# Kernel tuning notes

Hardware: AMD Instinct MI355X
Metric: run time of the kernel (lower is better)

Reference implementation:

```python
import jax, jax.numpy as jnp
import numpy as np
import math

N, D, E, M, MODS = 16384, 1024, 5, 64, 5
K = 1  # top-k for sparse router


def setup_inputs() -> dict:
    key = jax.random.key(0)
    ks = jax.random.split(key, 24)
    rn = lambda k, shape, s=1.0: jax.random.normal(k, shape, dtype=jnp.float32) * s
    inp = {
        'x': rn(ks[0], (N, D)),
        'spectrogram': rn(ks[1], (N, D)),
        'waveform': rn(ks[2], (N, D)),
        'pitch': rn(ks[3], (N, D)),
        'envelope': rn(ks[4], (N, D)),
        'phase': rn(ks[5], (N, D)),
        # routers (torch Linear: y = x @ W.T + b, W is [out,in]); init std=0.01
        'Wsoft': rn(ks[6], (E, D), 0.01), 'bsoft': jnp.zeros((E,), jnp.float32),
        'Wsparse': rn(ks[7], (E, D), 0.01), 'bsparse': jnp.zeros((E,), jnp.float32),
        # memory (plain randn, not re-initialized)
        'm_key': rn(ks[8], (M, D)), 'm_val': rn(ks[9], (M, E)),
        # experts: Linear(D,D) -> SiLU -> Linear(D,D), stacked over E
        'W1': rn(ks[10], (E, D, D), 0.01), 'b1': jnp.zeros((E, D), jnp.float32),
        'W2': rn(ks[11], (E, D, D), 0.01), 'b2': jnp.zeros((E, D), jnp.float32),
        # fusion gates: Linear(D,1) + sigmoid, one per modality
        'Wg': rn(ks[12], (MODS, D), 0.01), 'bg': jnp.zeros((MODS,), jnp.float32),
        # fusion projection: Linear(D*MODS, D)
        'Wf': rn(ks[13], (D, D * MODS), 0.01), 'bf': jnp.zeros((D,), jnp.float32),
    }
    return inp


def reference(x, spectrogram, waveform, pitch, envelope, phase,
              Wsoft, bsoft, Wsparse, bsparse, m_key, m_val,
              W1, b1, W2, b2, Wg, bg, Wf, bf):
    alpha_moe = jnp.float32(0.5)
    alpha_fusion = jnp.float32(0.5)

    # soft router: softmax(Linear)
    soft_w = jax.nn.softmax(x @ Wsoft.T + bsoft, axis=-1)          # [N,E]

    # sparse router: top-k + softmax, scattered back to [N,E]
    logits = x @ Wsparse.T + bsparse                               # [N,E]
    top_vals, top_idx = jax.lax.top_k(logits, K)                   # [N,K]
    sparse_gates = jax.nn.softmax(top_vals, axis=-1)               # [N,K]
    one_hot = jax.nn.one_hot(top_idx, E, dtype=logits.dtype)       # [N,K,E]
    sparse_w = jnp.sum(one_hot * sparse_gates[..., None], axis=1)  # [N,E]

    # memory-augmented gating
    attn = jax.nn.softmax((x @ m_key.T) / math.sqrt(D), axis=-1)   # [N,M]
    memory_w = jax.nn.softmax(attn @ m_val, axis=-1)               # [N,E]

    mixed_w = alpha_moe * sparse_w + (1 - alpha_moe) * soft_w
    final_w = (mixed_w + memory_w) / 2                             # [N,E]

    # dense all-expert MLP: [N,E,D]
    h = jax.nn.silu(jnp.einsum('nd,eod->neo', x, W1) + b1)
    expert_out = jnp.einsum('ned,eod->neo', h, W2) + b2
    moe_output = jnp.einsum('neo,ne->no', expert_out, final_w)     # [N,D]

    # gated multimodal fusion
    features = [spectrogram, waveform, pitch, envelope, phase]
    gates = jax.nn.sigmoid(x @ Wg.T + bg)                          # [N,MODS]
    scaled = [gates[:, q:q + 1] * features[q] for q in range(MODS)]
    fused = jnp.concatenate(scaled, axis=-1) @ Wf.T + bf           # [N,D]

    return alpha_fusion * fused + (1 - alpha_fusion) * moe_output
```

## Files before the change

kernel.cpp:

```cpp
#include <hip/hip_runtime.h>
#include <stdint.h>

typedef __bf16 bf16x8 __attribute__((ext_vector_type(8)));
typedef float f32x4 __attribute__((ext_vector_type(4)));
typedef unsigned short u16;
typedef u16 ushort8 __attribute__((ext_vector_type(8)));
typedef u16 ushort4v __attribute__((ext_vector_type(4)));

__device__ __forceinline__ u16 f2bf(float f) {
    uint32_t u = __builtin_bit_cast(uint32_t, f);
    u += 0x7FFFu + ((u >> 16) & 1u);
    return (u16)(u >> 16);
}

__device__ __forceinline__ void gload16(const void* g, void* l) {
    __builtin_amdgcn_global_load_lds(
        reinterpret_cast<const __attribute__((address_space(1))) void*>(reinterpret_cast<uintptr_t>(g)),
        reinterpret_cast<__attribute__((address_space(3))) void*>(reinterpret_cast<uintptr_t>(l)),
        16, 0, 0);
}

#define BAR() asm volatile("s_barrier" ::: "memory")
#define SGBi(m, n) __builtin_amdgcn_sched_group_barrier((m), (n), 0)

template <int V>
__device__ __forceinline__ void sgb_q() {
    SGBi(0x70, V);
    SGBi(0x8, 2); SGBi(0x100, 1);
    SGBi(0x8, 2); SGBi(0x100, 1);
    SGBi(0x8, 2); SGBi(0x100, 1);
    SGBi(0x8, 2); SGBi(0x100, 1);
    SGBi(0x8, 8);
}
__device__ __forceinline__ void sgb_q3() {
    SGBi(0x70, 2);
    SGBi(0x8, 1); SGBi(0x100, 1);
    SGBi(0x8, 1); SGBi(0x100, 1);
    SGBi(0x8, 1); SGBi(0x100, 1);
    SGBi(0x8, 1); SGBi(0x100, 1);
    SGBi(0x8, 12);
    SGBi(0x100, 8);
}

template <int MODE>
__global__ __launch_bounds__(512, 2)
void gemm256(const u16* __restrict__ A, int lda,
             const u16* __restrict__ B, int ldb, int K,
             void* __restrict__ Cout, int ldc,
             const float* __restrict__ bias, const float* __restrict__ fw05,
             const float* __restrict__ g05,
             const float* __restrict__ f0, const float* __restrict__ f1,
             const float* __restrict__ f2, const float* __restrict__ f3,
             const float* __restrict__ f4)
{
    __shared__ __align__(16) u16 As[2 * 256 * 64];
    __shared__ __align__(16) u16 Bs[2 * 256 * 64];

    const int t    = threadIdx.x;
    const int lane = t & 63;
    const int wave = t >> 6;
    const int l16  = lane & 15;
    const int lhi  = lane >> 4;
    const int wm   = wave >> 2;
    const int wn   = wave & 3;

    const int gx  = gridDim.x;
    const int nwg = gx * gridDim.y;
    int id  = blockIdx.y * gx + blockIdx.x;
    int swz = (nwg & 7) ? id : ((id & 7) * (nwg >> 3) + (id >> 3));
    const int bx = swz % gx;
    const int by = swz / gx;

    const size_t rowBase = (size_t)by * 256;
    const int    colBase = bx * 256;
    const int    NT      = K >> 6;

    const int rl0 = t >> 3;
    const int ko0 = (t & 7) * 8;
    const int kos = ((t & 7) ^ (rl0 & 7)) * 8;

    const u16* aRow = A + (rowBase + rl0) * (size_t)lda + kos;
    const u16* bRow = B + (size_t)(colBase + rl0) * ldb + kos;
    u16* asW = As + rl0 * 64 + ko0;
    u16* bsW = Bs + rl0 * 64 + ko0;

#define STA(bufo, e, r0, r1)                                                     \
    do {                                                                         \
        gload16(aRow + (size_t)(r0) * lda + (e), asW + (bufo) + (r0) * 64);      \
        gload16(aRow + (size_t)(r1) * lda + (e), asW + (bufo) + (r1) * 64);      \
    } while (0)
#define STB(bufo, e, b0)                                                         \
    do {                                                                         \
        gload16(bRow + (size_t)(b0) * ldb + (e), bsW + (bufo) + (b0) * 64);      \
        gload16(bRow + (size_t)((b0) + 64) * ldb + (e),                          \
                bsW + (bufo) + ((b0) + 64) * 64);                                \
    } while (0)

    const int sw = l16 & 7;
    const u16* aRd0 = As + (wm * 128 + l16) * 64 + ((lhi ^ sw) * 8);
    const u16* aRd1 = As + (wm * 128 + l16) * 64 + (((lhi + 4) ^ sw) * 8);
    const u16* bRd0 = Bs + (wn * 64 + l16) * 64 + ((lhi ^ sw) * 8);
    const u16* bRd1 = Bs + (wn * 64 + l16) * 64 + (((lhi + 4) ^ sw) * 8);

#define RDAF(dst, cc, qq)                                                        \
    do {                                                                         \
        dst[0][0] = *(const bf16x8*)(aRd0 + (cc) + (2 * (qq) + 0) * 1024);       \
        dst[0][1] = *(const bf16x8*)(aRd1 + (cc) + (2 * (qq) + 0) * 1024);       \
        dst[1][0] = *(const bf16x8*)(aRd0 + (cc) + (2 * (qq) + 1) * 1024);       \
        dst[1][1] = *(const bf16x8*)(aRd1 + (cc) + (2 * (qq) + 1) * 1024);       \
    } while (0)
#define RDB(cc)                                                                  \
    do {                                                                         \
        _Pragma("unroll")                                                        \
        for (int ni = 0; ni < 4; ++ni) {                                         \
            bfr[ni][0] = *(const bf16x8*)(bRd0 + (cc) + ni * 1024);              \
            bfr[ni][1] = *(const bf16x8*)(bRd1 + (cc) + ni * 1024);              \
        }                                                                        \
    } while (0)
#define MMX(af, r0)                                                              \
    do {                                                                         \
        __builtin_amdgcn_s_setprio(1);                                           \
        _Pragma("unroll")                                                        \
        for (int s = 0; s < 2; ++s)                                              \
            _Pragma("unroll")                                                    \
            for (int ni = 0; ni < 4; ++ni)                                       \
                _Pragma("unroll")                                                \
                for (int kk = 0; kk < 2; ++kk)                                   \
                    acc[(r0) + s][ni] = __builtin_amdgcn_mfma_f32_16x16x32_bf16( \
                        af[s][kk], bfr[ni][kk], acc[(r0) + s][ni], 0, 0, 0);     \
        __builtin_amdgcn_s_setprio(0);                                           \
    } while (0)

    f32x4 acc[8][4];
#pragma unroll
    for (int i = 0; i < 8; i++)
#pragma unroll
        for (int j = 0; j < 4; j++)
            acc[i][j] = (f32x4){0.f, 0.f, 0.f, 0.f};

    const float* fsrc = nullptr;
    int   dbase = 0;
    f32x4 bl0 = {0.f, 0.f, 0.f, 0.f}, bl1 = {0.f, 0.f, 0.f, 0.f};
    float bgd = 0.f;
    if constexpr (MODE == 0) {
        const int qm = bx >> 2;
        fsrc  = (qm == 0) ? f0 : (qm == 1) ? f1 : (qm == 2) ? f2 : (qm == 3) ? f3 : f4;
        dbase = (bx & 3) * 256;
        const int br = t >> 5, bc = (t & 31) * 8;
        bl0 = *(const f32x4*)(fsrc + (rowBase + br) * 1024 + dbase + bc);
        bl1 = *(const f32x4*)(fsrc + (rowBase + br) * 1024 + dbase + bc + 4);
        bgd = g05[(rowBase + br) * 5 + (bx >> 2)];
    }

    STA(0, 0, 0, 128);
    STA(0, 0, 64, 192);
    STB(0, 0, 0);
    STB(0, 0, 128);
    STB(16384, 64, 0);
    STB(16384, 64, 128);
    STA(16384, 64, 0, 128);
    asm volatile("s_waitcnt vmcnt(6)" ::: "memory");
    BAR();

    bf16x8 afA[2][2], afB[2][2], bfr[4][2];
    RDAF(afA, 0, 0);
    RDB(0);

    for (int tt = 0; tt < NT; ++tt) {
        const int c  = (tt & 1) << 14;
        const int cn = c ^ 16384;
        const int e1 = ((tt + 1 < NT) ? tt + 1 : NT - 1) << 6;
        const int e2 = ((tt + 2 < NT) ? tt + 2 : NT - 1) << 6;

        if constexpr (MODE == 0) {
            const int idx = tt * 512 + t;
            const int br  = idx >> 5;
            const int bc  = (idx & 31) * 8;
            ushort8 bv;
            bv[0] = f2bf(bgd * bl0[0]); bv[1] = f2bf(bgd * bl0[1]);
            bv[2] = f2bf(bgd * bl0[2]); bv[3] = f2bf(bgd * bl0[3]);
            bv[4] = f2bf(bgd * bl1[0]); bv[5] = f2bf(bgd * bl1[1]);
            bv[6] = f2bf(bgd * bl1[2]); bv[7] = f2bf(bgd * bl1[3]);
            *(ushort8*)((u16*)Cout + (rowBase + br) * (size_t)ldc
                        + 5184 + colBase + bc) = bv;
            const int t2   = (tt + 1 < 16) ? tt + 1 : 15;
            const int idx2 = t2 * 512 + t;
            const int br2  = idx2 >> 5;
            const int bc2  = (idx2 & 31) * 8;
            bl0 = *(const f32x4*)(fsrc + (rowBase + br2) * 1024 + dbase + bc2);
            bl1 = *(const f32x4*)(fsrc + (rowBase + br2) * 1024 + dbase + bc2 + 4);
            bgd = g05[(rowBase + br2) * 5 + (bx >> 2)];
        }
        STA(cn, e1, 64, 192);
        RDAF(afB, c, 1);
        MMX(afA, 0);
        sgb_q<(MODE == 0) ? 6 : 2>();
        BAR();

        STB(c, e2, 0);
        RDAF(afA, c, 2);
        MMX(afB, 2);
        sgb_q<2>();
        BAR();

        STB(c, e2, 128);
        RDAF(afB, c, 3);
        MMX(afA, 4);
        sgb_q<2>();
        asm volatile("s_waitcnt vmcnt(4)" ::: "memory");
        BAR();

        STA(c, e2, 0, 128);
        RDAF(afA, cn, 0);
        MMX(afB, 6);
        RDB(cn);
        sgb_q3();
        BAR();
    }

    const int orow = wm * 128 + lhi * 4;
    const int ocol = colBase + wn * 64 + l16;

    if constexpr (MODE == 0) {
        u16* C = (u16*)Cout;
        const int eidx = colBase >> 10;
#pragma unroll
        for (int mi = 0; mi < 8; mi++) {
#pragma unroll
            for (int j = 0; j < 4; j++) {
                size_t r = rowBase + orow + mi * 16 + j;
                float w = fw05[r * 5 + eidx];
#pragma unroll
                for (int ni = 0; ni < 4; ni++) {
                    int cc = ocol + ni * 16;
                    float v = acc[mi][ni][j] + bias[cc];
                    float s = v / (1.f + __expf(-v));
                    C[r * (size_t)ldc + cc] = f2bf(w * s);
                }
            }
        }
    } else {
        float* C = (float*)Cout;
#pragma unroll
        for (int mi = 0; mi < 8; mi++) {
#pragma unroll
            for (int j = 0; j < 4; j++) {
                size_t r = rowBase + orow + mi * 16 + j;
#pragma unroll
                for (int ni = 0; ni < 4; ni++) {
                    size_t idx = r * (size_t)ldc + (ocol + ni * 16);
                    C[idx] = acc[mi][ni][j];
                }
            }
        }
    }
#undef STA
#undef STB
#undef RDAF
#undef RDB
#undef MMX
}

__global__ __launch_bounds__(256)
void router_kernel(const float* __restrict__ x,
                   const float* __restrict__ Wsoft, const float* __restrict__ Wsparse,
                   const float* __restrict__ m_key, const float* __restrict__ Wg,
                   float* __restrict__ logits, u16* __restrict__ Xbf)
{
    __shared__ float Xs[128][66];
    __shared__ float Ws[80][132];

    const int t    = threadIdx.x;
    const int lane = t & 63;
    const int wave = t >> 6;
    const int row0 = blockIdx.x * 64;

    float acc[20];
#pragma unroll
    for (int c = 0; c < 20; c++) acc[c] = 0.f;

    for (int k0 = 0; k0 < 1024; k0 += 128) {
#pragma unroll
        for (int i = 0; i < 8; i++) {
            int f4 = i * 256 + t;
            int r  = f4 >> 5;
            int kk = (f4 & 31) * 4;
            f32x4 v = *(const f32x4*)(x + (size_t)(row0 + r) * 1024 + k0 + kk);
            Xs[kk + 0][r] = v[0]; Xs[kk + 1][r] = v[1];
            Xs[kk + 2][r] = v[2]; Xs[kk + 3][r] = v[3];
            ushort4v o4;
            o4[0] = f2bf(v[0]); o4[1] = f2bf(v[1]);
            o4[2] = f2bf(v[2]); o4[3] = f2bf(v[3]);
            *(ushort4v*)(Xbf + (size_t)(row0 + r) * 1024 + k0 + kk) = o4;
        }
#pragma unroll
        for (int i = 0; i < 10; i++) {
            int f4 = i * 256 + t;
            int j  = f4 >> 5;
            int kk = (f4 & 31) * 4;
            const float* src;
            if      (j < 5)  src = Wsoft   + (size_t)j * 1024;
            else if (j < 10) src = Wsparse + (size_t)(j - 5) * 1024;
            else if (j < 74) src = m_key   + (size_t)(j - 10) * 1024;
            else             src = Wg      + (size_t)(j - 74) * 1024;
            *(f32x4*)&Ws[j][kk] = *(const f32x4*)(src + k0 + kk);
        }
        __syncthreads();

        for (int k4 = 0; k4 < 32; k4++) {
            float x0 = Xs[k4 * 4 + 0][lane];
            float x1 = Xs[k4 * 4 + 1][lane];
            float x2 = Xs[k4 * 4 + 2][lane];
            float x3 = Xs[k4 * 4 + 3][lane];
#pragma unroll
            for (int c = 0; c < 20; c++) {
                f32x4 w = *(const f32x4*)&Ws[wave * 20 + c][k4 * 4];
                acc[c] += x0 * w[0] + x1 * w[1] + x2 * w[2] + x3 * w[3];
            }
        }
        __syncthreads();
    }

    float* dst = logits + (size_t)(row0 + lane) * 80 + wave * 20;
#pragma unroll
    for (int c = 0; c < 20; c++) dst[c] = acc[c];
}

__global__ __launch_bounds__(256)
void finalize_kernel(const float* __restrict__ logits, const float* __restrict__ m_val,
                     const float* __restrict__ bsoft, const float* __restrict__ bsparse,
                     const float* __restrict__ bg,
                     float* __restrict__ fw05, float* __restrict__ g05,
                     u16* __restrict__ Abuf, int NC)
{
    __shared__ float mv[320];
    for (int i = threadIdx.x; i < 320; i += 256) mv[i] = m_val[i];
    __syncthreads();

    int idx = blockIdx.x * 256 + threadIdx.x;
    if (idx >= NC) return;
    const float* L = logits + (size_t)idx * 80;

    float sl[5];
#pragma unroll
    for (int e = 0; e < 5; e++) sl[e] = L[e] + bsoft[e];
    float sm = sl[0];
#pragma unroll
    for (int e = 1; e < 5; e++) sm = fmaxf(sm, sl[e]);
    float ssum = 0.f, sw[5];
#pragma unroll
    for (int e = 0; e < 5; e++) { sw[e] = __expf(sl[e] - sm); ssum += sw[e]; }
    float sinv = 1.f / ssum;

    int am = 0; float bv = L[5] + bsparse[0];
#pragma unroll
    for (int e = 1; e < 5; e++) {
        float v = L[5 + e] + bsparse[e];
        if (v > bv) { bv = v; am = e; }
    }

    float amax = -1e30f;
    for (int m = 0; m < 64; m++) amax = fmaxf(amax, L[10 + m] * 0.03125f);
    float asum = 0.f, mw[5] = {0.f, 0.f, 0.f, 0.f, 0.f};
    for (int m = 0; m < 64; m++) {
        float a = __expf(L[10 + m] * 0.03125f - amax);
        asum += a;
#pragma unroll
        for (int e = 0; e < 5; e++) mw[e] += a * mv[m * 5 + e];
    }
    float ainv = 1.f / asum;
#pragma unroll
    for (int e = 0; e < 5; e++) mw[e] *= ainv;
    float mm = mw[0];
#pragma unroll
    for (int e = 1; e < 5; e++) mm = fmaxf(mm, mw[e]);
    float msum = 0.f, me[5];
#pragma unroll
    for (int e = 0; e < 5; e++) { me[e] = __expf(mw[e] - mm); msum += me[e]; }
    float minv = 1.f / msum;

    u16* ta = Abuf + (size_t)idx * 10368;
#pragma unroll
    for (int e = 0; e < 5; e++) {
        float fv = 0.125f * ((e == am) ? 1.f : 0.f) + 0.125f * sw[e] * sinv
                 + 0.25f * me[e] * minv;
        fw05[(size_t)idx * 5 + e] = fv;
        ta[5120 + e] = f2bf(fv);
    }
#pragma unroll
    for (int q = 0; q < 5; q++)
        g05[(size_t)idx * 5 + q] = 0.5f / (1.f + __expf(-(L[74 + q] + bg[q])));

    for (int j = 5125; j < 5184; j++) ta[j] = 0;
    ta[10304] = f2bf(0.5f);
    for (int j = 10305; j < 10368; j++) ta[j] = 0;
}

__global__ __launch_bounds__(256)
void cast_bf16_kernel(const float* __restrict__ src, u16* __restrict__ dst, size_t n)
{
    size_t i = ((size_t)blockIdx.x * 256 + threadIdx.x) * 8;
    if (i >= n) return;
    f32x4 a = *(const f32x4*)(src + i);
    f32x4 b = *(const f32x4*)(src + i + 4);
    ushort8 o;
    o[0] = f2bf(a[0]); o[1] = f2bf(a[1]); o[2] = f2bf(a[2]); o[3] = f2bf(a[3]);
    o[4] = f2bf(b[0]); o[5] = f2bf(b[1]); o[6] = f2bf(b[2]); o[7] = f2bf(b[3]);
    *(ushort8*)(dst + i) = o;
}

__global__ __launch_bounds__(256)
void prep_wcat(const float* __restrict__ W2, const float* __restrict__ b2,
               const float* __restrict__ Wf, const float* __restrict__ bfias,
               u16* __restrict__ out)
{
    size_t tid = (size_t)blockIdx.x * 256 + threadIdx.x;
    int o  = (int)(tid / 1296);
    int c0 = (int)(tid % 1296) * 8;
    ushort8 v;
    if (c0 + 8 <= 5120) {
        int e = c0 >> 10, d = c0 & 1023;
        const float* s = W2 + ((size_t)e * 1024 + o) * 1024 + d;
        f32x4 a = *(const f32x4*)s;
        f32x4 b = *(const f32x4*)(s + 4);
        v[0] = f2bf(a[0]); v[1] = f2bf(a[1]); v[2] = f2bf(a[2]); v[3] = f2bf(a[3]);
        v[4] = f2bf(b[0]); v[5] = f2bf(b[1]); v[6] = f2bf(b[2]); v[7] = f2bf(b[3]);
    } else if (c0 < 5184) {
#pragma unroll
        for (int jj = 0; jj < 8; jj++) {
            int c = c0 + jj;
            float f = (c >= 5120 && c < 5125) ? b2[(size_t)(c - 5120) * 1024 + o] : 0.f;
            v[jj] = f2bf(f);
        }
    } else {
        int c2 = c0 - 5184;
        if (c2 + 8 <= 5120) {
            const float* s = Wf + (size_t)o * 5120 + c2;
            f32x4 a = *(const f32x4*)s;
            f32x4 b = *(const f32x4*)(s + 4);
            v[0] = f2bf(a[0]); v[1] = f2bf(a[1]); v[2] = f2bf(a[2]); v[3] = f2bf(a[3]);
            v[4] = f2bf(b[0]); v[5] = f2bf(b[1]); v[6] = f2bf(b[2]); v[7] = f2bf(b[3]);
        } else {
#pragma unroll
            for (int jj = 0; jj < 8; jj++) {
                int cj = c2 + jj;
                v[jj] = f2bf((cj == 5120) ? bfias[o] : 0.f);
            }
        }
    }
    *(ushort8*)(out + (size_t)o * 10368 + c0) = v;
}

extern "C" void kernel_launch(void* const* d_in, const int* in_sizes, int n_in,
                              void* d_out, int out_size, void* d_ws, size_t ws_size,
                              hipStream_t stream)
{
    (void)in_sizes; (void)n_in; (void)out_size;

    const float* x      = (const float*)d_in[0];
    const float* spect  = (const float*)d_in[1];
    const float* wavef  = (const float*)d_in[2];
    const float* pitch  = (const float*)d_in[3];
    const float* envel  = (const float*)d_in[4];
    const float* phase  = (const float*)d_in[5];
    const float* Wsoft  = (const float*)d_in[6];
    const float* bsoft  = (const float*)d_in[7];
    const float* Wsparse= (const float*)d_in[8];
    const float* bsparse= (const float*)d_in[9];
    const float* m_key  = (const float*)d_in[10];
    const float* m_val  = (const float*)d_in[11];
    const float* W1     = (const float*)d_in[12];
    const float* b1     = (const float*)d_in[13];
    const float* W2     = (const float*)d_in[14];
    const float* b2     = (const float*)d_in[15];
    const float* Wg     = (const float*)d_in[16];
    const float* bg     = (const float*)d_in[17];
    const float* Wf     = (const float*)d_in[18];
    const float* bfias  = (const float*)d_in[19];
    float* out = (float*)d_out;

    const int N = 16384;

    size_t fixed = (size_t)5 * 1024 * 1024 * 2 + (size_t)1024 * 10368 * 2;
    int NC = 16384;
    while (NC > 256 && fixed + (size_t)NC * 23144 > ws_size) NC >>= 1;

    char* p = (char*)d_ws;
    u16* W1bf = (u16*)p; p += (size_t)5 * 1024 * 1024 * 2;
    u16* Wcat = (u16*)p; p += (size_t)1024 * 10368 * 2;
    u16* Xbf  = (u16*)p; p += (size_t)NC * 1024 * 2;
    u16* Abuf = (u16*)p; p += (size_t)NC * 10368 * 2;
    float* logits = (float*)p; p += (size_t)NC * 80 * 4;
    float* fw05   = (float*)p; p += (size_t)NC * 5 * 4;
    float* g05    = (float*)p; p += (size_t)NC * 5 * 4;

    cast_bf16_kernel<<<2560, 256, 0, stream>>>(W1, W1bf, (size_t)5 * 1024 * 1024);
    prep_wcat<<<5184, 256, 0, stream>>>(W2, b2, Wf, bfias, Wcat);

    for (int n0 = 0; n0 < N; n0 += NC) {
        const size_t off = (size_t)n0 * 1024;

        router_kernel<<<NC / 64, 256, 0, stream>>>(x + off, Wsoft, Wsparse, m_key, Wg,
                                                   logits, Xbf);
        finalize_kernel<<<(NC + 255) / 256, 256, 0, stream>>>(
            logits, m_val, bsoft, bsparse, bg, fw05, g05, Abuf, NC);

        gemm256<0><<<dim3(20, NC / 256), 512, 0, stream>>>(
            Xbf, 1024, W1bf, 1024, 1024, Abuf, 10368, b1, fw05, g05,
            spect + off, wavef + off, pitch + off, envel + off, phase + off);

        gemm256<1><<<dim3(4, NC / 256), 512, 0, stream>>>(
            Abuf, 10368, Wcat, 10368, 10368, out + off, 1024,
            nullptr, nullptr, nullptr, nullptr, nullptr, nullptr, nullptr, nullptr);
    }
}
```

Baseline: 665.7 us.

## Offload modality gate-scale copy to dedicated producer waves in first GEMM

Splits the templated GEMM into two kernels. In the first, two extra waves (640 threads per block) convert the gated modality features to bf16 and write them into the concatenated activation buffer, work that the MFMA waves previously interleaved into their main loop. The extra waves join every block barrier so they stay in step with the GEMM waves. This takes global loads and stores off the MFMA waves' critical path, but launch bounds fall from two blocks per CU to one, which cuts occupancy and may raise register pressure.

After: 1.307 ms. 1.96x slower.

```diff
diff --git a/kernel.cpp b/kernel.cpp
--- a/kernel.cpp
+++ b/kernel.cpp
@@ -42,27 +42,19 @@
     SGBi(0x100, 8);
 }
 
-template <int MODE>
-__global__ __launch_bounds__(512, 2)
-void gemm256(const u16* __restrict__ A, int lda,
-             const u16* __restrict__ B, int ldb, int K,
-             void* __restrict__ Cout, int ldc,
-             const float* __restrict__ bias, const float* __restrict__ fw05,
-             const float* __restrict__ g05,
-             const float* __restrict__ f0, const float* __restrict__ f1,
-             const float* __restrict__ f2, const float* __restrict__ f3,
-             const float* __restrict__ f4)
+__global__ __launch_bounds__(640, 1)
+void gemm_moe(const u16* __restrict__ A, const u16* __restrict__ B,
+              u16* __restrict__ C, const float* __restrict__ bias,
+              const float* __restrict__ fw05, const float* __restrict__ g05,
+              const float* __restrict__ f0, const float* __restrict__ f1,
+              const float* __restrict__ f2, const float* __restrict__ f3,
+              const float* __restrict__ f4)
 {
     __shared__ __align__(16) u16 As[2 * 256 * 64];
     __shared__ __align__(16) u16 Bs[2 * 256 * 64];
 
     const int t    = threadIdx.x;
-    const int lane = t & 63;
     const int wave = t >> 6;
-    const int l16  = lane & 15;
-    const int lhi  = lane >> 4;
-    const int wm   = wave >> 2;
-    const int wn   = wave & 3;
 
     const int gx  = gridDim.x;
     const int nwg = gx * gridDim.y;
@@ -73,34 +65,44 @@
 
     const size_t rowBase = (size_t)by * 256;
     const int    colBase = bx * 256;
-    const int    NT      = K >> 6;
-
-    const int rl0 = t >> 3;
-    const int ko0 = (t & 7) * 8;
-    const int kos = ((t & 7) ^ (rl0 & 7)) * 8;
-
-    const u16* aRow = A + (rowBase + rl0) * (size_t)lda + kos;
-    const u16* bRow = B + (size_t)(colBase + rl0) * ldb + kos;
-    u16* asW = As + rl0 * 64 + ko0;
-    u16* bsW = Bs + rl0 * 64 + ko0;
+    const int    qm      = bx >> 2;
+    const float* fq = (qm == 0) ? f0 : (qm == 1) ? f1 : (qm == 2) ? f2
+                      : (qm == 3) ? f3 : f4;
+    const int dbase = (bx & 3) * 256;
+
+    if (wave < 8) {
+        const int lane = t & 63;
+        const int l16  = lane & 15;
+        const int lhi  = lane >> 4;
+        const int wm   = wave >> 2;
+        const int wn   = wave & 3;
+
+        const int rl0 = t >> 3;
+        const int ko0 = (t & 7) * 8;
+        const int kos = ((t & 7) ^ (rl0 & 7)) * 8;
+
+        const u16* aRow = A + (rowBase + rl0) * (size_t)1024 + kos;
+        const u16* bRow = B + (size_t)(colBase + rl0) * 1024 + kos;
+        u16* asW = As + rl0 * 64 + ko0;
+        u16* bsW = Bs + rl0 * 64 + ko0;
 
 #define STA(bufo, e, r0, r1)                                                     \
     do {                                                                         \
-        gload16(aRow + (size_t)(r0) * lda + (e), asW + (bufo) + (r0) * 64);      \
-        gload16(aRow + (size_t)(r1) * lda + (e), asW + (bufo) + (r1) * 64);      \
+        gload16(aRow + (size_t)(r0) * 1024 + (e), asW + (bufo) + (r0) * 64);     \
+        gload16(aRow + (size_t)(r1) * 1024 + (e), asW + (bufo) + (r1) * 64);     \
     } while (0)
 #define STB(bufo, e, b0)                                                         \
     do {                                                                         \
-        gload16(bRow + (size_t)(b0) * ldb + (e), bsW + (bufo) + (b0) * 64);      \
-        gload16(bRow + (size_t)((b0) + 64) * ldb + (e),                          \
+        gload16(bRow + (size_t)(b0) * 1024 + (e), bsW + (bufo) + (b0) * 64);     \
+        gload16(bRow + (size_t)((b0) + 64) * 1024 + (e),                         \
                 bsW + (bufo) + ((b0) + 64) * 64);                                \
     } while (0)
 
-    const int sw = l16 & 7;
-    const u16* aRd0 = As + (wm * 128 + l16) * 64 + ((lhi ^ sw) * 8);
-    const u16* aRd1 = As + (wm * 128 + l16) * 64 + (((lhi + 4) ^ sw) * 8);
-    const u16* bRd0 = Bs + (wn * 64 + l16) * 64 + ((lhi ^ sw) * 8);
-    const u16* bRd1 = Bs + (wn * 64 + l16) * 64 + (((lhi + 4) ^ sw) * 8);
+        const int sw = l16 & 7;
+        const u16* aRd0 = As + (wm * 128 + l16) * 64 + ((lhi ^ sw) * 8);
+        const u16* aRd1 = As + (wm * 128 + l16) * 64 + (((lhi + 4) ^ sw) * 8);
+        const u16* bRd0 = Bs + (wn * 64 + l16) * 64 + ((lhi ^ sw) * 8);
+        const u16* bRd1 = Bs + (wn * 64 + l16) * 64 + (((lhi + 4) ^ sw) * 8);
 
 #define RDAF(dst, cc, qq)                                                        \
     do {                                                                         \
@@ -131,26 +133,200 @@
         __builtin_amdgcn_s_setprio(0);                                           \
     } while (0)
 
+        f32x4 acc[8][4];
+#pragma unroll
+        for (int i = 0; i < 8; i++)
+#pragma unroll
+            for (int j = 0; j < 4; j++)
+                acc[i][j] = (f32x4){0.f, 0.f, 0.f, 0.f};
+
+        STA(0, 0, 0, 128);
+        STA(0, 0, 64, 192);
+        STB(0, 0, 0);
+        STB(0, 0, 128);
+        STB(16384, 64, 0);
+        STB(16384, 64, 128);
+        STA(16384, 64, 0, 128);
+        asm volatile("s_waitcnt vmcnt(6)" ::: "memory");
+        BAR();
+
+        bf16x8 afA[2][2], afB[2][2], bfr[4][2];
+        RDAF(afA, 0, 0);
+        RDB(0);
+
+        for (int tt = 0; tt < 16; ++tt) {
+            const int c  = (tt & 1) << 14;
+            const int cn = c ^ 16384;
+            const int e1 = ((tt + 1 < 16) ? tt + 1 : 15) << 6;
+            const int e2 = ((tt + 2 < 16) ? tt + 2 : 15) << 6;
+
+            STA(cn, e1, 64, 192);
+            RDAF(afB, c, 1);
+            MMX(afA, 0);
+            sgb_q<2>();
+            BAR();
+            STB(c, e2, 0);
+            RDAF(afA, c, 2);
+            MMX(afB, 2);
+            sgb_q<2>();
+            BAR();
+            STB(c, e2, 128);
+            RDAF(afB, c, 3);
+            MMX(afA, 4);
+            sgb_q<2>();
+            asm volatile("s_waitcnt vmcnt(4)" ::: "memory");
+            BAR();
+            STA(c, e2, 0, 128);
+            RDAF(afA, cn, 0);
+            MMX(afB, 6);
+            RDB(cn);
+            sgb_q3();
+            BAR();
+        }
+
+        const int orow = wm * 128 + lhi * 4;
+        const int ocol = colBase + wn * 64 + l16;
+#pragma unroll
+        for (int mi = 0; mi < 8; mi++) {
+#pragma unroll
+            for (int j = 0; j < 4; j++) {
+                size_t r = rowBase + orow + mi * 16 + j;
+                float w = fw05[r * 5 + qm];
+#pragma unroll
+                for (int ni = 0; ni < 4; ni++) {
+                    int cc = ocol + ni * 16;
+                    float v = acc[mi][ni][j] + bias[cc];
+                    float s = v / (1.f + __expf(-v));
+                    C[r * (size_t)10368 + cc] = f2bf(w * s);
+                }
+            }
+        }
+#undef STA
+#undef STB
+#undef RDAF
+#undef RDB
+#undef MMX
+    } else {
+        const int bt   = t - 512;
+        const int rof  = bt >> 5;
+        const int bcol = (bt & 31) * 8;
+
+        size_t r0 = rowBase + rof;
+        f32x4 la  = *(const f32x4*)(fq + r0 * 1024 + dbase + bcol);
+        f32x4 lb  = *(const f32x4*)(fq + r0 * 1024 + dbase + bcol + 4);
+        float lg  = g05[r0 * 5 + qm];
+        size_t rcur = r0;
+
+        BAR();
+
+        for (int s = 0; s < 64; ++s) {
+            ushort8 v;
+            v[0] = f2bf(lg * la[0]); v[1] = f2bf(lg * la[1]);
+            v[2] = f2bf(lg * la[2]); v[3] = f2bf(lg * la[3]);
+            v[4] = f2bf(lg * lb[0]); v[5] = f2bf(lg * lb[1]);
+            v[6] = f2bf(lg * lb[2]); v[7] = f2bf(lg * lb[3]);
+            *(ushort8*)(C + rcur * 10368 + 5184 + colBase + bcol) = v;
+
+            const int s2 = (s + 1 < 64) ? s + 1 : 63;
+            size_t rn = rowBase + s2 * 4 + rof;
+            la = *(const f32x4*)(fq + rn * 1024 + dbase + bcol);
+            lb = *(const f32x4*)(fq + rn * 1024 + dbase + bcol + 4);
+            lg = g05[rn * 5 + qm];
+            rcur = rn;
+            BAR();
+        }
+    }
+}
+
+__global__ __launch_bounds__(512, 2)
+void gemm_out(const u16* __restrict__ A, int lda,
+              const u16* __restrict__ B, int ldb, int K,
+              float* __restrict__ C, int ldc)
+{
+    __shared__ __align__(16) u16 As[2 * 256 * 64];
+    __shared__ __align__(16) u16 Bs[2 * 256 * 64];
+
+    const int t    = threadIdx.x;
+    const int lane = t & 63;
+    const int wave = t >> 6;
+    const int l16  = lane & 15;
+    const int lhi  = lane >> 4;
+    const int wm   = wave >> 2;
+    const int wn   = wave & 3;
+
+    const int gx  = gridDim.x;
+    const int nwg = gx * gridDim.y;
+    int id  = blockIdx.y * gx + blockIdx.x;
+    int swz = (nwg & 7) ? id : ((id & 7) * (nwg >> 3) + (id >> 3));
+    const int bx = swz % gx;
+    const int by = swz / gx;
+
+    const size_t rowBase = (size_t)by * 256;
+    const int    colBase = bx * 256;
+    const int    NT      = K >> 6;
+
+    const int rl0 = t >> 3;
+    const int ko0 = (t & 7) * 8;
+    const int kos = ((t & 7) ^ (rl0 & 7)) * 8;
+
+    const u16* aRow = A + (rowBase + rl0) * (size_t)lda + kos;
+    const u16* bRow = B + (size_t)(colBase + rl0) * ldb + kos;
+    u16* asW = As + rl0 * 64 + ko0;
+    u16* bsW = Bs + rl0 * 64 + ko0;
+
+#define STA(bufo, e, r0, r1)                                                     \
+    do {                                                                         \
+        gload16(aRow + (size_t)(r0) * lda + (e), asW + (bufo) + (r0) * 64);      \
+        gload16(aRow + (size_t)(r1) * lda + (e), asW + (bufo) + (r1) * 64);      \
+    } while (0)
+#define STB(bufo, e, b0)                                                         \
+    do {                                                                         \
+        gload16(bRow + (size_t)(b0) * ldb + (e), bsW + (bufo) + (b0) * 64);      \
+        gload16(bRow + (size_t)((b0) + 64) * ldb + (e),                          \
+                bsW + (bufo) + ((b0) + 64) * 64);                                \
+    } while (0)
+
+    const int sw = l16 & 7;
+    const u16* aRd0 = As + (wm * 128 + l16) * 64 + ((lhi ^ sw) * 8);
+    const u16* aRd1 = As + (wm * 128 + l16) * 64 + (((lhi + 4) ^ sw) * 8);
+    const u16* bRd0 = Bs + (wn * 64 + l16) * 64 + ((lhi ^ sw) * 8);
+    const u16* bRd1 = Bs + (wn * 64 + l16) * 64 + (((lhi + 4) ^ sw) * 8);
+
+#define RDAF(dst, cc, qq)                                                        \
+    do {                                                                         \
+        dst[0][0] = *(const bf16x8*)(aRd0 + (cc) + (2 * (qq) + 0) * 1024);       \
+        dst[0][1] = *(const bf16x8*)(aRd1 + (cc) + (2 * (qq) + 0) * 1024);       \
+        dst[1][0] = *(const bf16x8*)(aRd0 + (cc) + (2 * (qq) + 1) * 1024);       \
+        dst[1][1] = *(const bf16x8*)(aRd1 + (cc) + (2 * (qq) + 1) * 1024);       \
+    } while (0)
+#define RDB(cc)                                                                  \
+    do {                                                                         \
+        _Pragma("unroll")                                                        \
+        for (int ni = 0; ni < 4; ++ni) {                                         \
+            bfr[ni][0] = *(const bf16x8*)(bRd0 + (cc) + ni * 1024);              \
+            bfr[ni][1] = *(const bf16x8*)(bRd1 + (cc) + ni * 1024);              \
+        }                                                                        \
+    } while (0)
+#define MMX(af, r0)                                                              \
+    do {                                                                         \
+        __builtin_amdgcn_s_setprio(1);                                           \
+        _Pragma("unroll")                                                        \
+        for (int s = 0; s < 2; ++s)                                              \
+            _Pragma("unroll")                                                    \
+            for (int ni = 0; ni < 4; ++ni)                                       \
+                _Pragma("unroll")                                                \
+                for (int kk = 0; kk < 2; ++kk)                                   \
+                    acc[(r0) + s][ni] = __builtin_amdgcn_mfma_f32_16x16x32_bf16( \
+                        af[s][kk], bfr[ni][kk], acc[(r0) + s][ni], 0, 0, 0);     \
+        __builtin_amdgcn_s_setprio(0);                                           \
+    } while (0)
+
     f32x4 acc[8][4];
 #pragma unroll
     for (int i = 0; i < 8; i++)
 #pragma unroll
         for (int j = 0; j < 4; j++)
             acc[i][j] = (f32x4){0.f, 0.f, 0.f, 0.f};
-
-    const float* fsrc = nullptr;
-    int   dbase = 0;
-    f32x4 bl0 = {0.f, 0.f, 0.f, 0.f}, bl1 = {0.f, 0.f, 0.f, 0.f};
-    float bgd = 0.f;
-    if constexpr (MODE == 0) {
-        const int qm = bx >> 2;
-        fsrc  = (qm == 0) ? f0 : (qm == 1) ? f1 : (qm == 2) ? f2 : (qm == 3) ? f3 : f4;
-        dbase = (bx & 3) * 256;
-        const int br = t >> 5, bc = (t & 31) * 8;
-        bl0 = *(const f32x4*)(fsrc + (rowBase + br) * 1024 + dbase + bc);
-        bl1 = *(const f32x4*)(fsrc + (rowBase + br) * 1024 + dbase + bc + 4);
-        bgd = g05[(rowBase + br) * 5 + (bx >> 2)];
-    }
 
     STA(0, 0, 0, 128);
     STA(0, 0, 64, 192);
@@ -172,29 +348,10 @@
         const int e1 = ((tt + 1 < NT) ? tt + 1 : NT - 1) << 6;
         const int e2 = ((tt + 2 < NT) ? tt + 2 : NT - 1) << 6;
 
-        if constexpr (MODE == 0) {
-            const int idx = tt * 512 + t;
-            const int br  = idx >> 5;
-            const int bc  = (idx & 31) * 8;
-            ushort8 bv;
-            bv[0] = f2bf(bgd * bl0[0]); bv[1] = f2bf(bgd * bl0[1]);
-            bv[2] = f2bf(bgd * bl0[2]); bv[3] = f2bf(bgd * bl0[3]);
-            bv[4] = f2bf(bgd * bl1[0]); bv[5] = f2bf(bgd * bl1[1]);
-            bv[6] = f2bf(bgd * bl1[2]); bv[7] = f2bf(bgd * bl1[3]);
-            *(ushort8*)((u16*)Cout + (rowBase + br) * (size_t)ldc
-                        + 5184 + colBase + bc) = bv;
-            const int t2   = (tt + 1 < 16) ? tt + 1 : 15;
-            const int idx2 = t2 * 512 + t;
-            const int br2  = idx2 >> 5;
-            const int bc2  = (idx2 & 31) * 8;
-            bl0 = *(const f32x4*)(fsrc + (rowBase + br2) * 1024 + dbase + bc2);
-            bl1 = *(const f32x4*)(fsrc + (rowBase + br2) * 1024 + dbase + bc2 + 4);
-            bgd = g05[(rowBase + br2) * 5 + (bx >> 2)];
-        }
         STA(cn, e1, 64, 192);
         RDAF(afB, c, 1);
         MMX(afA, 0);
-        sgb_q<(MODE == 0) ? 6 : 2>();
+        sgb_q<2>();
         BAR();
 
         STB(c, e2, 0);
@@ -220,37 +377,15 @@
 
     const int orow = wm * 128 + lhi * 4;
     const int ocol = colBase + wn * 64 + l16;
-
-    if constexpr (MODE == 0) {
-        u16* C = (u16*)Cout;
-        const int eidx = colBase >> 10;
-#pragma unroll
-        for (int mi = 0; mi < 8; mi++) {
-#pragma unroll
-            for (int j = 0; j < 4; j++) {
-                size_t r = rowBase + orow + mi * 16 + j;
-                float w = fw05[r * 5 + eidx];
-#pragma unroll
-                for (int ni = 0; ni < 4; ni++) {
-                    int cc = ocol + ni * 16;
-                    float v = acc[mi][ni][j] + bias[cc];
-                    float s = v / (1.f + __expf(-v));
-                    C[r * (size_t)ldc + cc] = f2bf(w * s);
-                }
-            }
-        }
-    } else {
-        float* C = (float*)Cout;
-#pragma unroll
-        for (int mi = 0; mi < 8; mi++) {
-#pragma unroll
-            for (int j = 0; j < 4; j++) {
-                size_t r = rowBase + orow + mi * 16 + j;
-#pragma unroll
-                for (int ni = 0; ni < 4; ni++) {
-                    size_t idx = r * (size_t)ldc + (ocol + ni * 16);
-                    C[idx] = acc[mi][ni][j];
-                }
+#pragma unroll
+    for (int mi = 0; mi < 8; mi++) {
+#pragma unroll
+        for (int j = 0; j < 4; j++) {
+            size_t r = rowBase + orow + mi * 16 + j;
+#pragma unroll
+            for (int ni = 0; ni < 4; ni++) {
+                size_t idx = r * (size_t)ldc + (ocol + ni * 16);
+                C[idx] = acc[mi][ni][j];
             }
         }
     }
@@ -505,12 +640,11 @@
         finalize_kernel<<<(NC + 255) / 256, 256, 0, stream>>>(
             logits, m_val, bsoft, bsparse, bg, fw05, g05, Abuf, NC);
 
-        gemm256<0><<<dim3(20, NC / 256), 512, 0, stream>>>(
-            Xbf, 1024, W1bf, 1024, 1024, Abuf, 10368, b1, fw05, g05,
+        gemm_moe<<<dim3(20, NC / 256), 640, 0, stream>>>(
+            Xbf, W1bf, Abuf, b1, fw05, g05,
             spect + off, wavef + off, pitch + off, envel + off, phase + off);
 
-        gemm256<1><<<dim3(4, NC / 256), 512, 0, stream>>>(
-            Abuf, 10368, Wcat, 10368, 10368, out + off, 1024,
-            nullptr, nullptr, nullptr, nullptr, nullptr, nullptr, nullptr, nullptr);
-    }
-}
+        gemm_out<<<dim3(4, NC / 256), 512, 0, stream>>>(
+            Abuf, 10368, Wcat, 10368, 10368, out + off, 1024);
+    }
+}
```
